# Performance work log

Hardware: AMD Instinct MI355X
Metric: run time of the kernel (lower is better)

Reference implementation:

```python
import jax, jax.numpy as jnp
import numpy as np
import math

BLOCK_SIZE = 64
GATE_HIDDEN = 128


def _rmsnorm(x, w, eps=1e-6):
    v = jnp.mean(jnp.square(x), axis=-1, keepdims=True)
    return x * jax.lax.rsqrt(v + eps) * w


def _rotate_half(x):
    x1, x2 = jnp.split(x, 2, axis=-1)
    return jnp.concatenate([-x2, x1], axis=-1)


def _rope(x, cos, sin):
    # x: [B, S, H, D]; cos/sin: [B, S, D] -> unsqueeze head dim (unsqueeze_dim=2)
    c = cos[:, :, None, :]
    s = sin[:, :, None, :]
    return x * c + _rotate_half(x) * s


def setup_inputs() -> dict:
    key = jax.random.key(0)
    ks = jax.random.split(key, 10)
    B, S, Hk, D = 4, 65536, 8, 128
    Hq, g, Dg = 32, 4, GATE_HIDDEN
    nb = S // BLOCK_SIZE
    xav_q = math.sqrt(6.0 / (D + Dg))
    xav_k = math.sqrt(6.0 / (2 * D + Dg))
    return {
        "k": jax.random.normal(ks[0], (B, S, Hk, D), jnp.float32),
        "q": jax.random.normal(ks[1], (B, 1, Hq, D), jnp.float32),
        "Wq": jax.random.uniform(ks[2], (Hk, g, D, Dg), jnp.float32, -xav_q, xav_q),
        "Wk": jax.random.uniform(ks[3], (Hk, 2 * D, Dg), jnp.float32, -xav_k, xav_k),
        "qnorm_w": jnp.ones((Dg,), jnp.float32),
        "knorm_w": jnp.ones((Dg,), jnp.float32),
        "cos_q": jax.random.uniform(ks[4], (B, 1, Dg), jnp.float32, -1.0, 1.0),
        "sin_q": jax.random.uniform(ks[5], (B, 1, Dg), jnp.float32, -1.0, 1.0),
        "cos_k": jax.random.uniform(ks[6], (B, nb, Dg), jnp.float32, -1.0, 1.0),
        "sin_k": jax.random.uniform(ks[7], (B, nb, Dg), jnp.float32, -1.0, 1.0),
        "attention_mask": jnp.ones((B, Hk, nb), jnp.bool_),
        "block_budget": 128,
    }


def reference(k, q, Wq, Wk, qnorm_w, knorm_w, cos_q, sin_q, cos_k, sin_k,
              attention_mask, block_budget):
    B, S, Hk, D = k.shape
    nb = S // BLOCK_SIZE
    g = q.shape[2] // Hk
    Dg = Wk.shape[-1]
    scale = 1.0 / math.sqrt(Dg)

    # --- K path: block pooling (avg + max) -> per-head linear -> RMSNorm -> RoPE
    kb = k.reshape(B, nb, BLOCK_SIZE, Hk, D)
    k_pooled = jnp.concatenate([kb.mean(axis=2), kb.max(axis=2)], axis=-1)  # [B,nb,Hk,2D]
    k_c = jnp.einsum('bshi,hio->bsho', k_pooled, Wk)                         # [B,nb,Hk,Dg]
    k_c = _rmsnorm(k_c, knorm_w)
    k_c = _rope(k_c, cos_k, sin_k)

    # --- Q path (Qproj): grouped per-k-head projection -> RMSNorm -> RoPE
    qg = q.reshape(B, 1, Hk, g, D)
    qp = jnp.einsum('bskgi,kgio->bsko', qg, Wq)                              # [B,1,Hk,Dg]
    qp = _rmsnorm(qp, qnorm_w)
    qp = _rope(qp, cos_q, sin_q)
    qv = qp[:, 0]                                                            # [B,Hk,Dg]

    # --- gate scores + softmax
    attn = jnp.einsum('bhd,bshd->bhs', qv, k_c) * scale                      # [B,Hk,nb]
    attn = jnp.where(attention_mask, attn, jnp.float32(-1e20))
    attn = jax.nn.softmax(attn, axis=-1)

    # --- token_budget sparse block mask: topk + scatter
    _, topk_idx = jax.lax.top_k(attn, block_budget)                          # [B,Hk,k]
    blk = jnp.arange(nb)
    mask = jnp.any(topk_idx[..., :, None] == blk[None, None, None, :], axis=-2)
    mask = mask & attention_mask
    mask = mask.at[:, :, -1].set(True)
    return mask
```

## Files before the change

kernel.cpp:

```cpp
#include <hip/hip_runtime.h>
#include <hip/hip_bf16.h>
#include <math.h>

#define NB   1024
#define HKH  8

typedef float f4 __attribute__((ext_vector_type(4)));

__global__ __launch_bounds__(512) void qproj_kernel(const float* __restrict__ q,
                                                    const float* __restrict__ Wq,
                                                    const float* __restrict__ qnw,
                                                    const float* __restrict__ cq,
                                                    const float* __restrict__ sq,
                                                    float* __restrict__ qv) {
    int b = blockIdx.x >> 3, h = blockIdx.x & 7;
    int t = threadIdx.x;
    int o = t & 127, seg = t >> 7;
    __shared__ float qs[512];
    __shared__ float part[4][128];
    __shared__ float red[2];
    __shared__ float ybuf[128];
    qs[t] = q[(size_t)b * 4096 + (size_t)h * 512 + t];
    __syncthreads();
    const float* wqp = Wq + (size_t)h * 512 * 128 + o;
    float acc = 0.0f;
    int g0 = seg * 128;
#pragma unroll 4
    for (int gi = g0; gi < g0 + 128; ++gi)
        acc = fmaf(qs[gi], wqp[(size_t)gi * 128], acc);
    part[seg][o] = acc;
    __syncthreads();
    if (t < 128) {
        float a = part[0][o] + part[1][o] + part[2][o] + part[3][o];
        ybuf[o] = a;
        float ss = a * a;
        for (int off = 32; off > 0; off >>= 1) ss += __shfl_xor(ss, off);
        if ((o & 63) == 0) red[o >> 6] = ss;
    }
    __syncthreads();
    if (t < 128) {
        float scale = rsqrtf((red[0] + red[1]) * (1.0f / 128.0f) + 1e-6f);
        float y  = ybuf[o] * scale * qnw[o];
        int op   = (o < 64) ? o + 64 : o - 64;
        float yp = ybuf[op] * scale * qnw[op];
        float rot = (o < 64) ? -yp : yp;
        qv[((size_t)b * HKH + h) * 128 + o] =
            fmaf(y, cq[b * 128 + o], rot * sq[b * 128 + o]);
    }
}

__global__ __launch_bounds__(256) void fused_kernel(const float* __restrict__ kin,
                                                    const float* __restrict__ Wk,
                                                    const float* __restrict__ knw,
                                                    const float* __restrict__ cosk,
                                                    const float* __restrict__ sink,
                                                    const float* __restrict__ qv,
                                                    float* __restrict__ scores) {
    __shared__ float At[256][32];
    int wg   = blockIdx.x;
    int tile = wg & 255;
    int b    = wg >> 8;
    int t    = threadIdx.x;
    int h    = t >> 5;
    int c    = t & 31;

    {
        const float inv = 1.0f / 64.0f;
#pragma unroll
        for (int bi = 0; bi < 4; ++bi) {
            size_t row0 = (size_t)b * 65536 + (size_t)tile * 256 + (size_t)bi * 64;
            const f4* src = (const f4*)kin + row0 * 256 + t;
            f4 v = __builtin_nontemporal_load(src);
            f4 s = v, m = v;
#pragma unroll 8
            for (int r = 1; r < 64; ++r) {
                f4 u = __builtin_nontemporal_load(src + (size_t)r * 256);
                s += u;
                m.x = fmaxf(m.x, u.x); m.y = fmaxf(m.y, u.y);
                m.z = fmaxf(m.z, u.z); m.w = fmaxf(m.w, u.w);
            }
#pragma unroll
            for (int j = 0; j < 4; ++j) {
                int k0 = c * 4 + j;
                int g  = (k0 >> 3) & 7;
                At[k0      ][((h ^ g) << 2) | bi] = s[j] * inv;
                At[k0 + 128][((h ^ g) << 2) | bi] = m[j];
            }
        }
    }
    __syncthreads();

    float acc[4][4];
#pragma unroll
    for (int i = 0; i < 4; ++i)
#pragma unroll
        for (int j = 0; j < 4; ++j) acc[i][j] = 0.0f;
    const float* wp = Wk + (size_t)h * 32768 + c * 4;
#pragma unroll 4
    for (int k = 0; k < 256; ++k) {
        int g = (k >> 3) & 7;
        f4 a = *(const f4*)&At[k][(h ^ g) << 2];
        f4 w = *(const f4*)(wp + (size_t)k * 128);
#pragma unroll
        for (int i = 0; i < 4; ++i) {
            acc[i][0] = fmaf(a[i], w.x, acc[i][0]);
            acc[i][1] = fmaf(a[i], w.y, acc[i][1]);
            acc[i][2] = fmaf(a[i], w.z, acc[i][2]);
            acc[i][3] = fmaf(a[i], w.w, acc[i][3]);
        }
    }

    f4 kn  = *(const f4*)(knw + c * 4);
    f4 qvr = *(const f4*)(qv + ((size_t)b * HKH + h) * 128 + c * 4);
#pragma unroll
    for (int i = 0; i < 4; ++i) {
        int blkg = tile * 4 + i;
        float ss = 0.0f;
#pragma unroll
        for (int j = 0; j < 4; ++j) ss = fmaf(acc[i][j], acc[i][j], ss);
#pragma unroll
        for (int off = 1; off < 32; off <<= 1) ss += __shfl_xor(ss, off);
        float scale = rsqrtf(ss * (1.0f / 128.0f) + 1e-6f);
        f4 cb = *(const f4*)(cosk + ((size_t)b * NB + blkg) * 128 + c * 4);
        f4 sb = *(const f4*)(sink + ((size_t)b * NB + blkg) * 128 + c * 4);
        float part = 0.0f;
#pragma unroll
        for (int j = 0; j < 4; ++j) {
            float y  = acc[i][j] * scale * kn[j];
            float yp = __shfl_xor(y, 16);
            float rot = (c < 16) ? -yp : yp;
            float z = fmaf(y, cb[j], rot * sb[j]);
            part = fmaf(z, qvr[j], part);
        }
#pragma unroll
        for (int off = 1; off < 32; off <<= 1) part += __shfl_xor(part, off);
        if (c == 0)
            scores[((size_t)b * HKH + h) * NB + blkg] = part * 0.08838834764831845f;
    }
}

__device__ inline bool read_mask(const void* amp, int mode, size_t idx) {
    if (mode == 1) return ((const int*)amp)[idx] != 0;
    if (mode == 2) return ((const unsigned int*)amp)[idx] != 0u;
    return ((const unsigned char*)amp)[idx] != 0;
}

__global__ __launch_bounds__(512) void topk_kernel(const float* __restrict__ scores,
                                                   const void* __restrict__ amraw,
                                                   const int* __restrict__ bbp,
                                                   int* __restrict__ out) {
    int b = blockIdx.x >> 3, h = blockIdx.x & 7;
    int t = threadIdx.x;
    __shared__ float sv[NB];
    __shared__ int mode_sh;

    if (t == 0) {
        const unsigned int* w = (const unsigned int*)amraw;
        bool allint = true, allflt = true;
        for (int i = 0; i < 64; ++i) {
            unsigned int x = w[i];
            if (x != 0u && x != 1u) allint = false;
            if (x != 0u && x != 0x3f800000u) allflt = false;
        }
        mode_sh = allint ? 1 : (allflt ? 2 : 0);
    }
    __syncthreads();
    int mode = mode_sh;
    size_t rowoff = ((size_t)b * HKH + h) * NB;
    const float* src = scores + rowoff;
    for (int s = t; s < NB; s += 512)
        sv[s] = read_mask(amraw, mode, rowoff + s) ? src[s] : -1e20f;
    __syncthreads();

    int bb = bbp[0];
    if (bb > NB) bb = NB;
    if (bb < 1)  bb = 1;

    int e0 = t, e1 = t + 512;
    float v0 = sv[e0], v1 = sv[e1];
    int r0 = 0, r1 = 0;
#pragma unroll 4
    for (int j4 = 0; j4 < 256; ++j4) {
        f4 w = *(const f4*)&sv[j4 * 4];
        int jb = j4 * 4;
        r0 += (w.x > v0) + (w.y > v0) + (w.z > v0) + (w.w > v0);
        r1 += (w.x > v1) + (w.y > v1) + (w.z > v1) + (w.w > v1);
        r0 += (w.x == v0 && jb + 0 < e0) + (w.y == v0 && jb + 1 < e0)
            + (w.z == v0 && jb + 2 < e0) + (w.w == v0 && jb + 3 < e0);
        r1 += (w.x == v1 && jb + 0 < e1) + (w.y == v1 && jb + 1 < e1)
            + (w.z == v1 && jb + 2 < e1) + (w.w == v1 && jb + 3 < e1);
    }
    int* dst = out + rowoff;
    bool am0 = read_mask(amraw, mode, rowoff + e0);
    bool am1 = read_mask(amraw, mode, rowoff + e1);
    dst[e0] = ((r0 < bb && am0)) ? 1 : 0;
    dst[e1] = ((r1 < bb && am1) || (e1 == NB - 1)) ? 1 : 0;
}

extern "C" void kernel_launch(void* const* d_in, const int* in_sizes, int n_in,
                              void* d_out, int out_size, void* d_ws, size_t ws_size,
                              hipStream_t stream) {
    (void)in_sizes; (void)n_in; (void)out_size; (void)ws_size;
    const float* k   = (const float*)d_in[0];
    const float* q   = (const float*)d_in[1];
    const float* Wq  = (const float*)d_in[2];
    const float* Wk  = (const float*)d_in[3];
    const float* qnw = (const float*)d_in[4];
    const float* knw = (const float*)d_in[5];
    const float* cq  = (const float*)d_in[6];
    const float* sq  = (const float*)d_in[7];
    const float* ck  = (const float*)d_in[8];
    const float* sk  = (const float*)d_in[9];
    const void*  am  = d_in[10];
    const int*   bb  = (const int*)d_in[11];
    int* out = (int*)d_out;

    float* qv     = (float*)d_ws;
    float* scores = qv + 4 * HKH * 128;

    qproj_kernel<<<32, 512, 0, stream>>>(q, Wq, qnw, cq, sq, qv);
    fused_kernel<<<1024, 256, 0, stream>>>(k, Wk, knw, ck, sk, qv, scores);
    topk_kernel<<<32, 512, 0, stream>>>(scores, am, bb, out);
}
```

Baseline: 258.1 us.

## Software-pipeline k pooling with Wk GEMM using double-buffered shared tiles

Each workgroup now handles four consecutive tiles instead of one, and the grid shrinks from 1024 to 256 blocks. The pooled-K buffer in shared memory is double-buffered so that streaming loads and pooling for the next tile interleave with the FMAs of the current tile's Wk projection. The goal is to hide the HBM streaming of k behind compute. In exchange, shared memory per block doubles and register pressure rises, and with only 256 workgroups on a 256-CU part occupancy may be too low to saturate memory bandwidth.

```diff
diff --git a/kernel.cpp b/kernel.cpp
--- a/kernel.cpp
+++ b/kernel.cpp
@@ -56,24 +56,25 @@
                                                     const float* __restrict__ sink,
                                                     const float* __restrict__ qv,
                                                     float* __restrict__ scores) {
-    __shared__ float At[256][32];
-    int wg   = blockIdx.x;
-    int tile = wg & 255;
-    int b    = wg >> 8;
-    int t    = threadIdx.x;
-    int h    = t >> 5;
-    int c    = t & 31;
+    __shared__ float At[2][256][32];
+    int wg  = blockIdx.x;
+    int b   = wg >> 6;
+    int grp = wg & 63;
+    int t   = threadIdx.x;
+    int h   = t >> 5;
+    int c   = t & 31;
+    const float inv = 1.0f / 64.0f;
 
     {
-        const float inv = 1.0f / 64.0f;
+        int tile = grp * 4;
 #pragma unroll
         for (int bi = 0; bi < 4; ++bi) {
             size_t row0 = (size_t)b * 65536 + (size_t)tile * 256 + (size_t)bi * 64;
             const f4* src = (const f4*)kin + row0 * 256 + t;
-            f4 v = __builtin_nontemporal_load(src);
-            f4 s = v, m = v;
+            f4 s = {0.f, 0.f, 0.f, 0.f};
+            f4 m = {-3.4e38f, -3.4e38f, -3.4e38f, -3.4e38f};
 #pragma unroll 8
-            for (int r = 1; r < 64; ++r) {
+            for (int r = 0; r < 64; ++r) {
                 f4 u = __builtin_nontemporal_load(src + (size_t)r * 256);
                 s += u;
                 m.x = fmaxf(m.x, u.x); m.y = fmaxf(m.y, u.y);
@@ -83,59 +84,101 @@
             for (int j = 0; j < 4; ++j) {
                 int k0 = c * 4 + j;
                 int g  = (k0 >> 3) & 7;
-                At[k0      ][((h ^ g) << 2) | bi] = s[j] * inv;
-                At[k0 + 128][((h ^ g) << 2) | bi] = m[j];
-            }
-        }
-    }
-    __syncthreads();
-
-    float acc[4][4];
-#pragma unroll
-    for (int i = 0; i < 4; ++i)
-#pragma unroll
-        for (int j = 0; j < 4; ++j) acc[i][j] = 0.0f;
+                At[0][k0      ][((h ^ g) << 2) | bi] = s[j] * inv;
+                At[0][k0 + 128][((h ^ g) << 2) | bi] = m[j];
+            }
+        }
+    }
+
     const float* wp = Wk + (size_t)h * 32768 + c * 4;
-#pragma unroll 4
-    for (int k = 0; k < 256; ++k) {
-        int g = (k >> 3) & 7;
-        f4 a = *(const f4*)&At[k][(h ^ g) << 2];
-        f4 w = *(const f4*)(wp + (size_t)k * 128);
-#pragma unroll
-        for (int i = 0; i < 4; ++i) {
-            acc[i][0] = fmaf(a[i], w.x, acc[i][0]);
-            acc[i][1] = fmaf(a[i], w.y, acc[i][1]);
-            acc[i][2] = fmaf(a[i], w.z, acc[i][2]);
-            acc[i][3] = fmaf(a[i], w.w, acc[i][3]);
-        }
-    }
-
     f4 kn  = *(const f4*)(knw + c * 4);
     f4 qvr = *(const f4*)(qv + ((size_t)b * HKH + h) * 128 + c * 4);
-#pragma unroll
-    for (int i = 0; i < 4; ++i) {
-        int blkg = tile * 4 + i;
-        float ss = 0.0f;
-#pragma unroll
-        for (int j = 0; j < 4; ++j) ss = fmaf(acc[i][j], acc[i][j], ss);
-#pragma unroll
-        for (int off = 1; off < 32; off <<= 1) ss += __shfl_xor(ss, off);
-        float scale = rsqrtf(ss * (1.0f / 128.0f) + 1e-6f);
-        f4 cb = *(const f4*)(cosk + ((size_t)b * NB + blkg) * 128 + c * 4);
-        f4 sb = *(const f4*)(sink + ((size_t)b * NB + blkg) * 128 + c * 4);
-        float part = 0.0f;
-#pragma unroll
-        for (int j = 0; j < 4; ++j) {
-            float y  = acc[i][j] * scale * kn[j];
-            float yp = __shfl_xor(y, 16);
-            float rot = (c < 16) ? -yp : yp;
-            float z = fmaf(y, cb[j], rot * sb[j]);
-            part = fmaf(z, qvr[j], part);
-        }
-#pragma unroll
-        for (int off = 1; off < 32; off <<= 1) part += __shfl_xor(part, off);
-        if (c == 0)
-            scores[((size_t)b * HKH + h) * NB + blkg] = part * 0.08838834764831845f;
+
+    for (int it = 0; it < 4; ++it) {
+        __syncthreads();
+        int cur = it & 1, nxt = cur ^ 1;
+        float acc[4][4];
+#pragma unroll
+        for (int i = 0; i < 4; ++i)
+#pragma unroll
+            for (int j = 0; j < 4; ++j) acc[i][j] = 0.0f;
+
+        if (it < 3) {
+            int tile = grp * 4 + it + 1;
+#pragma unroll
+            for (int bi = 0; bi < 4; ++bi) {
+                size_t row0 = (size_t)b * 65536 + (size_t)tile * 256 + (size_t)bi * 64;
+                const f4* src = (const f4*)kin + row0 * 256 + t;
+                f4 s = {0.f, 0.f, 0.f, 0.f};
+                f4 m = {-3.4e38f, -3.4e38f, -3.4e38f, -3.4e38f};
+#pragma unroll 4
+                for (int r = 0; r < 64; ++r) {
+                    f4 u = __builtin_nontemporal_load(src + (size_t)r * 256);
+                    s += u;
+                    m.x = fmaxf(m.x, u.x); m.y = fmaxf(m.y, u.y);
+                    m.z = fmaxf(m.z, u.z); m.w = fmaxf(m.w, u.w);
+                    int k = bi * 64 + r;
+                    int g = (k >> 3) & 7;
+                    f4 a = *(const f4*)&At[cur][k][(h ^ g) << 2];
+                    f4 w = *(const f4*)(wp + (size_t)k * 128);
+#pragma unroll
+                    for (int i = 0; i < 4; ++i) {
+                        acc[i][0] = fmaf(a[i], w.x, acc[i][0]);
+                        acc[i][1] = fmaf(a[i], w.y, acc[i][1]);
+                        acc[i][2] = fmaf(a[i], w.z, acc[i][2]);
+                        acc[i][3] = fmaf(a[i], w.w, acc[i][3]);
+                    }
+                }
+#pragma unroll
+                for (int j = 0; j < 4; ++j) {
+                    int k0 = c * 4 + j;
+                    int g  = (k0 >> 3) & 7;
+                    At[nxt][k0      ][((h ^ g) << 2) | bi] = s[j] * inv;
+                    At[nxt][k0 + 128][((h ^ g) << 2) | bi] = m[j];
+                }
+            }
+        } else {
+#pragma unroll 4
+            for (int k = 0; k < 256; ++k) {
+                int g = (k >> 3) & 7;
+                f4 a = *(const f4*)&At[cur][k][(h ^ g) << 2];
+                f4 w = *(const f4*)(wp + (size_t)k * 128);
+#pragma unroll
+                for (int i = 0; i < 4; ++i) {
+                    acc[i][0] = fmaf(a[i], w.x, acc[i][0]);
+                    acc[i][1] = fmaf(a[i], w.y, acc[i][1]);
+                    acc[i][2] = fmaf(a[i], w.z, acc[i][2]);
+                    acc[i][3] = fmaf(a[i], w.w, acc[i][3]);
+                }
+            }
+        }
+
+        int tileg = grp * 4 + it;
+#pragma unroll
+        for (int i = 0; i < 4; ++i) {
+            int blkg = tileg * 4 + i;
+            float ss = 0.0f;
+#pragma unroll
+            for (int j = 0; j < 4; ++j) ss = fmaf(acc[i][j], acc[i][j], ss);
+#pragma unroll
+            for (int off = 1; off < 32; off <<= 1) ss += __shfl_xor(ss, off);
+            float scale = rsqrtf(ss * (1.0f / 128.0f) + 1e-6f);
+            f4 cb = *(const f4*)(cosk + ((size_t)b * NB + blkg) * 128 + c * 4);
+            f4 sb = *(const f4*)(sink + ((size_t)b * NB + blkg) * 128 + c * 4);
+            float part = 0.0f;
+#pragma unroll
+            for (int j = 0; j < 4; ++j) {
+                float y  = acc[i][j] * scale * kn[j];
+                float yp = __shfl_xor(y, 16);
+                float rot = (c < 16) ? -yp : yp;
+                float z = fmaf(y, cb[j], rot * sb[j]);
+                part = fmaf(z, qvr[j], part);
+            }
+#pragma unroll
+            for (int off = 1; off < 32; off <<= 1) part += __shfl_xor(part, off);
+            if (c == 0)
+                scores[((size_t)b * HKH + h) * NB + blkg] = part * 0.08838834764831845f;
+        }
     }
 }
 
@@ -219,6 +262,6 @@
     float* scores = qv + 4 * HKH * 128;
 
     qproj_kernel<<<32, 512, 0, stream>>>(q, Wq, qnw, cq, sq, qv);
-    fused_kernel<<<1024, 256, 0, stream>>>(k, Wk, knw, ck, sk, qv, scores);
+    fused_kernel<<<256, 256, 0, stream>>>(k, Wk, knw, ck, sk, qv, scores);
     topk_kernel<<<32, 512, 0, stream>>>(scores, am, bb, out);
 }
```

New measurement: 271.3 us. 1.05x slower.

## Warp-specialize fused kernel into producer pooling and consumer GEMM waves

Applied to the files above, without the earlier changes.

Restructures the fused pooling/projection kernel into 768-thread workgroups. Each one has 512 producer threads that stream and pool K into a 4-stage shared buffer, and 256 consumer threads that spin on shared-memory counters and run the Wk projection, RMSNorm, RoPE and score dot product. The aim is to overlap the memory-bound pooling with the compute of earlier tiles and to reuse Wk across 16 blocks per workgroup. The grid shrinks from 1024 to 256 workgroups, which cuts parallelism on the HBM stream. Spin-waiting wastes issue slots, and the larger shared footprint may lower occupancy.

```diff
diff --git a/kernel.cpp b/kernel.cpp
--- a/kernel.cpp
+++ b/kernel.cpp
@@ -4,6 +4,8 @@
 
 #define NB   1024
 #define HKH  8
+#define NPROD 512
+#define NCONS 256
 
 typedef float f4 __attribute__((ext_vector_type(4)));
 
@@ -49,93 +51,115 @@
     }
 }
 
-__global__ __launch_bounds__(256) void fused_kernel(const float* __restrict__ kin,
+__global__ __launch_bounds__(768) void fused_kernel(const float* __restrict__ kin,
                                                     const float* __restrict__ Wk,
                                                     const float* __restrict__ knw,
                                                     const float* __restrict__ cosk,
                                                     const float* __restrict__ sink,
                                                     const float* __restrict__ qv,
                                                     float* __restrict__ scores) {
-    __shared__ float At[256][32];
-    int wg   = blockIdx.x;
-    int tile = wg & 255;
-    int b    = wg >> 8;
-    int t    = threadIdx.x;
-    int h    = t >> 5;
-    int c    = t & 31;
-
-    {
+    __shared__ float At[4][256][32];
+    __shared__ int produced[4];
+    int wg  = blockIdx.x;
+    int b   = wg >> 6;
+    int grp = wg & 63;
+    int t   = threadIdx.x;
+
+    if (t < 4) produced[t] = 0;
+    __syncthreads();
+
+    if (t < NPROD) {
+        int col = t & 255;
+        int h   = col >> 5;
+        int c   = col & 31;
+        int bihalf = t >> 8;
         const float inv = 1.0f / 64.0f;
-#pragma unroll
-        for (int bi = 0; bi < 4; ++bi) {
-            size_t row0 = (size_t)b * 65536 + (size_t)tile * 256 + (size_t)bi * 64;
-            const f4* src = (const f4*)kin + row0 * 256 + t;
-            f4 v = __builtin_nontemporal_load(src);
-            f4 s = v, m = v;
+        for (int it = 0; it < 4; ++it) {
+#pragma unroll
+            for (int bb2 = 0; bb2 < 2; ++bb2) {
+                int bi = bihalf + bb2 * 2;
+                size_t row0 = (size_t)b * 65536 +
+                              ((size_t)grp * 16 + it * 4 + bi) * 64;
+                const f4* src = (const f4*)kin + row0 * 256 + col;
+                f4 s = {0.f, 0.f, 0.f, 0.f};
+                f4 m = {-3.4e38f, -3.4e38f, -3.4e38f, -3.4e38f};
 #pragma unroll 8
-            for (int r = 1; r < 64; ++r) {
-                f4 u = __builtin_nontemporal_load(src + (size_t)r * 256);
-                s += u;
-                m.x = fmaxf(m.x, u.x); m.y = fmaxf(m.y, u.y);
-                m.z = fmaxf(m.z, u.z); m.w = fmaxf(m.w, u.w);
+                for (int r = 0; r < 64; ++r) {
+                    f4 u = __builtin_nontemporal_load(src + (size_t)r * 256);
+                    s += u;
+                    m.x = fmaxf(m.x, u.x); m.y = fmaxf(m.y, u.y);
+                    m.z = fmaxf(m.z, u.z); m.w = fmaxf(m.w, u.w);
+                }
+#pragma unroll
+                for (int j = 0; j < 4; ++j) {
+                    int k0 = c * 4 + j;
+                    int g  = (k0 >> 3) & 7;
+                    At[it][k0      ][((h ^ g) << 2) | bi] = s[j] * inv;
+                    At[it][k0 + 128][((h ^ g) << 2) | bi] = m[j];
+                }
             }
-#pragma unroll
-            for (int j = 0; j < 4; ++j) {
-                int k0 = c * 4 + j;
-                int g  = (k0 >> 3) & 7;
-                At[k0      ][((h ^ g) << 2) | bi] = s[j] * inv;
-                At[k0 + 128][((h ^ g) << 2) | bi] = m[j];
+            __threadfence_block();
+            atomicAdd(&produced[it], 1);
+        }
+    } else {
+        int tc = t - NPROD;
+        int h  = tc >> 5;
+        int c  = tc & 31;
+        const float* wp = Wk + (size_t)h * 32768 + c * 4;
+        f4 kn  = *(const f4*)(knw + c * 4);
+        f4 qvr = *(const f4*)(qv + ((size_t)b * HKH + h) * 128 + c * 4);
+        volatile int* vfl = (volatile int*)produced;
+
+        for (int it = 0; it < 4; ++it) {
+            while (vfl[it] < NPROD) __builtin_amdgcn_s_sleep(2);
+            __threadfence_block();
+
+            float acc[4][4];
+#pragma unroll
+            for (int i = 0; i < 4; ++i)
+#pragma unroll
+                for (int j = 0; j < 4; ++j) acc[i][j] = 0.0f;
+#pragma unroll 4
+            for (int k = 0; k < 256; ++k) {
+                int g = (k >> 3) & 7;
+                f4 a = *(const f4*)&At[it][k][(h ^ g) << 2];
+                f4 w = *(const f4*)(wp + (size_t)k * 128);
+#pragma unroll
+                for (int i = 0; i < 4; ++i) {
+                    acc[i][0] = fmaf(a[i], w.x, acc[i][0]);
+                    acc[i][1] = fmaf(a[i], w.y, acc[i][1]);
+                    acc[i][2] = fmaf(a[i], w.z, acc[i][2]);
+                    acc[i][3] = fmaf(a[i], w.w, acc[i][3]);
+                }
+            }
+
+#pragma unroll
+            for (int i = 0; i < 4; ++i) {
+                int blkg = (grp * 16 + it * 4) + i;
+                float ss = 0.0f;
+#pragma unroll
+                for (int j = 0; j < 4; ++j) ss = fmaf(acc[i][j], acc[i][j], ss);
+#pragma unroll
+                for (int off = 1; off < 32; off <<= 1) ss += __shfl_xor(ss, off);
+                float scale = rsqrtf(ss * (1.0f / 128.0f) + 1e-6f);
+                f4 cb = *(const f4*)(cosk + ((size_t)b * NB + blkg) * 128 + c * 4);
+                f4 sb = *(const f4*)(sink + ((size_t)b * NB + blkg) * 128 + c * 4);
+                float part = 0.0f;
+#pragma unroll
+                for (int j = 0; j < 4; ++j) {
+                    float y  = acc[i][j] * scale * kn[j];
+                    float yp = __shfl_xor(y, 16);
+                    float rot = (c < 16) ? -yp : yp;
+                    float z = fmaf(y, cb[j], rot * sb[j]);
+                    part = fmaf(z, qvr[j], part);
+                }
+#pragma unroll
+                for (int off = 1; off < 32; off <<= 1) part += __shfl_xor(part, off);
+                if (c == 0)
+                    scores[((size_t)b * HKH + h) * NB + blkg] =
+                        part * 0.08838834764831845f;
             }
         }
-    }
-    __syncthreads();
-
-    float acc[4][4];
-#pragma unroll
-    for (int i = 0; i < 4; ++i)
-#pragma unroll
-        for (int j = 0; j < 4; ++j) acc[i][j] = 0.0f;
-    const float* wp = Wk + (size_t)h * 32768 + c * 4;
-#pragma unroll 4
-    for (int k = 0; k < 256; ++k) {
-        int g = (k >> 3) & 7;
-        f4 a = *(const f4*)&At[k][(h ^ g) << 2];
-        f4 w = *(const f4*)(wp + (size_t)k * 128);
-#pragma unroll
-        for (int i = 0; i < 4; ++i) {
-            acc[i][0] = fmaf(a[i], w.x, acc[i][0]);
-            acc[i][1] = fmaf(a[i], w.y, acc[i][1]);
-            acc[i][2] = fmaf(a[i], w.z, acc[i][2]);
-            acc[i][3] = fmaf(a[i], w.w, acc[i][3]);
-        }
-    }
-
-    f4 kn  = *(const f4*)(knw + c * 4);
-    f4 qvr = *(const f4*)(qv + ((size_t)b * HKH + h) * 128 + c * 4);
-#pragma unroll
-    for (int i = 0; i < 4; ++i) {
-        int blkg = tile * 4 + i;
-        float ss = 0.0f;
-#pragma unroll
-        for (int j = 0; j < 4; ++j) ss = fmaf(acc[i][j], acc[i][j], ss);
-#pragma unroll
-        for (int off = 1; off < 32; off <<= 1) ss += __shfl_xor(ss, off);
-        float scale = rsqrtf(ss * (1.0f / 128.0f) + 1e-6f);
-        f4 cb = *(const f4*)(cosk + ((size_t)b * NB + blkg) * 128 + c * 4);
-        f4 sb = *(const f4*)(sink + ((size_t)b * NB + blkg) * 128 + c * 4);
-        float part = 0.0f;
-#pragma unroll
-        for (int j = 0; j < 4; ++j) {
-            float y  = acc[i][j] * scale * kn[j];
-            float yp = __shfl_xor(y, 16);
-            float rot = (c < 16) ? -yp : yp;
-            float z = fmaf(y, cb[j], rot * sb[j]);
-            part = fmaf(z, qvr[j], part);
-        }
-#pragma unroll
-        for (int off = 1; off < 32; off <<= 1) part += __shfl_xor(part, off);
-        if (c == 0)
-            scores[((size_t)b * HKH + h) * NB + blkg] = part * 0.08838834764831845f;
     }
 }
 
@@ -219,6 +243,6 @@
     float* scores = qv + 4 * HKH * 128;
 
     qproj_kernel<<<32, 512, 0, stream>>>(q, Wq, qnw, cq, sq, qv);
-    fused_kernel<<<1024, 256, 0, stream>>>(k, Wk, knw, ck, sk, qv, scores);
+    fused_kernel<<<256, 768, 0, stream>>>(k, Wk, knw, ck, sk, qv, scores);
     topk_kernel<<<32, 512, 0, stream>>>(scores, am, bb, out);
 }
```

Result: no change. 262.3 us (+1.7%).
